# Kernel tuning notes

Measured on AMD Instinct MI355X. Metric: run time of the kernel, lower is better.

Reference implementation:

```python
import jax, jax.numpy as jnp
import numpy as np

NUM_V = 20000
N_EDGES = 160000
IN_CH, OUT_CH = 16, 32
IN_ORDER = OUT_ORDER = MID_ORDER = 2
N_RINGS = 2
BAND_LIMIT = 2
NUM_SAMPLES = 7


def build_kernel_basis(n_in, n_out, bl):
    """Equivariant kernel basis [num_bases, 2*bl+1, 2*n_out+1, 2*n_in+1].
    Freq axis layout: [const, cos(t), sin(t), cos(2t), sin(2t), ...] matching precomp."""
    Din, Dout, F = 2 * n_in + 1, 2 * n_out + 1, 2 * bl + 1
    I = np.eye(2)
    E = np.array([[0., -1.], [1., 0.]])   # rotation by pi/2
    S = np.array([[1., 0.], [0., -1.]])   # reflection
    ES = E @ S
    sl = lambda m: slice(0, 1) if m == 0 else slice(2 * m - 1, 2 * m + 1)
    bases = []

    def add(f, cos_blk, sin_blk, m, n):
        if f > bl:
            return
        B = np.zeros((F, Dout, Din))
        if f == 0:
            B[0, sl(m), sl(n)] = cos_blk
        else:
            B[2 * f - 1, sl(m), sl(n)] = cos_blk
            B[2 * f, sl(m), sl(n)] = sin_blk
        bases.append(B)

    for m in range(n_out + 1):
        for n in range(n_in + 1):
            if m == 0 and n == 0:
                add(0, np.ones((1, 1)), None, 0, 0)
            elif n == 0:  # scalar -> order-m pair: R(m t) e1, R(m t) e2
                add(m, np.array([[1.], [0.]]), np.array([[0.], [1.]]), m, 0)
                add(m, np.array([[0.], [1.]]), np.array([[-1.], [0.]]), m, 0)
            elif m == 0:  # order-n pair -> scalar: rows of R(-n t)
                add(n, np.array([[1., 0.]]), np.array([[0., 1.]]), 0, n)
                add(n, np.array([[0., 1.]]), np.array([[-1., 0.]]), 0, n)
            else:
                d = m - n
                f = abs(d)
                sg = 1.0 if d >= 0 else -1.0
                add(f, I, sg * E, m, n)          # R(d t)
                add(f, E, -sg * I, m, n)         # R(d t + pi/2)
                add(m + n, S, ES, m, n)          # R((m+n) t) S
                add(m + n, ES, -S, m, n)         # R((m+n) t + pi/2) S
    return np.stack(bases).astype(np.float32)


def fourier_mats(order, n):
    th = 2 * np.pi * np.arange(n) / n
    cols = [np.ones(n)]
    for m in range(1, order + 1):
        cols += [np.cos(m * th), np.sin(m * th)]
    T = np.stack(cols, 1)                              # [n_samples, 2*order+1]
    scale = np.array([1.0] + [2.0] * (2 * order)) / n
    Tinv = (T * scale).T                               # [2*order+1, n_samples]
    return jnp.asarray(T, jnp.float32), jnp.asarray(Tinv, jnp.float32)


def rep_act(x, alpha, order):
    """Gauge transport: rotate order-m feature pairs by m*alpha. x: [E,C,2*order+1]."""
    parts = [x[:, :, :1]]
    for m in range(1, order + 1):
        c = jnp.cos(m * alpha)[:, None]
        s = jnp.sin(m * alpha)[:, None]
        a, b = x[:, :, 2 * m - 1], x[:, :, 2 * m]
        parts.append(jnp.stack([c * a - s * b, s * a + c * b], axis=-1))
    return jnp.concatenate(parts, axis=-1)


def gem_conv(x, edge_index, precomp, connection, K, W, b, in_order):
    src, dst = edge_index[1], edge_index[0]
    xt = rep_act(x[src], connection, in_order)               # [E, Cin, Din] gather + transport
    wk = jnp.einsum('bfij,broc->froicj', K, W)               # fold basis with ring weights (small)
    t = jnp.einsum('ecj,froicj->efroi', xt, wk)              # per-edge freq/ring responses
    msg = jnp.einsum('efr,efroi->eoi', precomp, t)           # [E, Cout, Dout]
    out = jax.ops.segment_sum(msg, dst, num_segments=NUM_V)  # scatter-add to vertices
    return out.at[:, :, 0].add(b)                            # bias on scalar component


def regular_relu(x, order):
    T, Tinv = fourier_mats(order, NUM_SAMPLES)
    s = jnp.einsum('vcd,sd->vcs', x, T)   # irrep -> regular samples
    return jnp.einsum('vcs,ds->vcd', jax.nn.relu(s), Tinv)


def setup_inputs() -> dict:
    key = jax.random.key(0)
    k = jax.random.split(key, 8)
    nb = build_kernel_basis(IN_ORDER, MID_ORDER, BAND_LIMIT).shape[0]  # 19
    Din = 2 * IN_ORDER + 1
    x = jax.random.normal(k[0], (NUM_V, IN_CH, Din), jnp.float32)
    edge_index = jax.random.randint(k[1], (2, N_EDGES), 0, NUM_V, dtype=jnp.int32)
    precomp = jax.random.normal(k[2], (N_EDGES, 2 * BAND_LIMIT + 1, N_RINGS), jnp.float32)
    connection = jax.random.uniform(k[3], (N_EDGES,), jnp.float32) * (2 * np.pi)
    W1 = jax.random.normal(k[4], (nb, N_RINGS, OUT_CH, IN_CH), jnp.float32) * 0.1
    W2 = jax.random.normal(k[5], (nb, N_RINGS, OUT_CH, OUT_CH), jnp.float32) * 0.05
    W_lin = jax.random.normal(k[6], (OUT_CH, IN_CH), jnp.float32) * 0.1
    zeros = lambda: jnp.zeros((OUT_CH,), jnp.float32)
    return {"x": x, "edge_index": edge_index, "precomp": precomp, "connection": connection,
            "W1": W1, "b1": zeros(), "W2": W2, "b2": zeros(), "W_lin": W_lin, "b_lin": zeros()}


def reference(x, edge_index, precomp, connection, W1, b1, W2, b2, W_lin, b_lin):
    K = jnp.asarray(build_kernel_basis(IN_ORDER, MID_ORDER, BAND_LIMIT))  # orders equal -> shared basis
    y = gem_conv(x, edge_index, precomp, connection, K, W1, b1, IN_ORDER)
    y = regular_relu(y, MID_ORDER)
    y = gem_conv(y, edge_index, precomp, connection, K, W2, b2, MID_ORDER)
    res = jnp.einsum('vcd,oc->vod', x, W_lin) + b_lin[None, :, None]  # 1x1 conv residual
    o = min(y.shape[2], res.shape[2])
    y = y.at[:, :, :o].add(res[:, :, :o])
    return regular_relu(y, OUT_ORDER)
```

## Files before the change

### kernel.cpp

```cpp
#include <hip/hip_runtime.h>
#include <hip/hip_bf16.h>
#include <cstdint>

#define NV     20000
#define NE     160000
#define IC1    16
#define OC     32
#define DIN    5
#define NSLOT  49
#define NOUT   160
struct SlotTables {
    int n;
    int b[64], f[64], i[64], j[64];
    float v[64];
};

constexpr SlotTables make_slots() {
    SlotTables T{};
    float K[19][5][5][5] = {};
    int nb = 0;
    const int BL = 2;
    auto add = [&](int f, const float (*cb)[2], const float (*sb)[2],
                   int m, int n) {
        if (f > BL) return;
        int r0 = (m == 0) ? 0 : (2 * m - 1), nr = (m == 0) ? 1 : 2;
        int c0 = (n == 0) ? 0 : (2 * n - 1), nc = (n == 0) ? 1 : 2;
        for (int a = 0; a < nr; a++)
            for (int bb = 0; bb < nc; bb++) {
                if (f == 0) {
                    K[nb][0][r0 + a][c0 + bb] = cb[a][bb];
                } else {
                    K[nb][2 * f - 1][r0 + a][c0 + bb] = cb[a][bb];
                    K[nb][2 * f    ][r0 + a][c0 + bb] = sb[a][bb];
                }
            }
        nb++;
    };
    const float ONE[2][2]  = {{1, 0}, {0, 0}};
    const float I2[2][2]   = {{1, 0}, {0, 1}};
    const float E2[2][2]   = {{0, -1}, {1, 0}};
    const float S2[2][2]   = {{1, 0}, {0, -1}};
    const float ES2[2][2]  = {{0, 1}, {1, 0}};
    const float NS2[2][2]  = {{-1, 0}, {0, 1}};
    const float C10[2][2]  = {{1, 0}, {0, 0}};
    const float C01[2][2]  = {{0, 0}, {1, 0}};
    const float CM10[2][2] = {{-1, 0}, {0, 0}};
    const float R10[2][2]  = {{1, 0}, {0, 0}};
    const float R01[2][2]  = {{0, 1}, {0, 0}};
    const float RM10[2][2] = {{-1, 0}, {0, 0}};

    for (int m = 0; m <= 2; m++)
        for (int n = 0; n <= 2; n++) {
            if (m == 0 && n == 0) {
                add(0, ONE, ONE, 0, 0);
            } else if (n == 0) {
                add(m, C10, C01, m, 0);
                add(m, C01, CM10, m, 0);
            } else if (m == 0) {
                add(n, R10, R01, 0, n);
                add(n, R01, RM10, 0, n);
            } else {
                int d = m - n;
                int f = d >= 0 ? d : -d;
                float sg = d >= 0 ? 1.f : -1.f;
                const float sgE[2][2]  = {{0, -sg}, {sg, 0}};
                const float msgI[2][2] = {{-sg, 0}, {0, -sg}};
                add(f, I2, sgE, m, n);
                add(f, E2, msgI, m, n);
                add(m + n, S2, ES2, m, n);
                add(m + n, ES2, NS2, m, n);
            }
        }
    T.n = 0;
    for (int i = 0; i < 5; i++)
        for (int b = 0; b < nb; b++)
            for (int f = 0; f < 5; f++)
                for (int j = 0; j < 5; j++)
                    if (K[b][f][i][j] != 0.0f) {
                        T.b[T.n] = b; T.f[T.n] = f; T.i[T.n] = i;
                        T.j[T.n] = j; T.v[T.n] = K[b][f][i][j];
                        T.n++;
                    }
    return T;
}

constexpr SlotTables SL = make_slots();
static_assert(SL.n == NSLOT, "expect 49 kernel-basis nonzeros");

__device__ __forceinline__ uint32_t bf16_rne(float f) {
    uint32_t u = __float_as_uint(f);
    u += 0x7fffu + ((u >> 16) & 1u);
    return u >> 16;
}

typedef __attribute__((ext_vector_type(8))) short bf16x8;
typedef __attribute__((ext_vector_type(4))) float f32x4;

template<int C>
__global__ __launch_bounds__(256) void build_M(const float* __restrict__ W,
                                               float* __restrict__ M) {
    int t = blockIdx.x * 256 + threadIdx.x;
    const int K = C * 50;
    if (t >= K * NOUT) return;
    int n = t % NOUT, k = t / NOUT;
    int o = n / 5, i = n % 5;
    int c = k / 50, r50 = k % 50;
    int j = r50 / 10, q = r50 % 10;
    int f = q >> 1, r = q & 1;
    float acc = 0.f;
    #pragma unroll
    for (int s = 0; s < NSLOT; s++) {
        if (SL.j[s] == j && SL.f[s] == f && SL.i[s] == i)
            acc += SL.v[s] * W[(size_t)((SL.b[s] * 2 + r) * 32 + o) * C + c];
    }
    M[(size_t)k * NOUT + n] = acc;
}

template<int K>
__global__ __launch_bounds__(256) void build_Mfrag(const float* __restrict__ M,
                                                   uint32_t* __restrict__ Mf) {
    int t = blockIdx.x * 256 + threadIdx.x;
    const int total = (K / 32) * 10 * 64 * 4;
    if (t >= total) return;
    int a = t & 3;
    int idx = t >> 2;
    int lane = idx & 63; idx >>= 6;
    int nt = idx % 10;
    int ck = idx / 10;
    int col = nt * 16 + (lane & 15);
    int k0 = ck * 32 + (lane >> 4) * 8 + 2 * a;
    uint32_t lo = bf16_rne(M[(size_t)k0 * NOUT + col]);
    uint32_t hi = bf16_rne(M[(size_t)(k0 + 1) * NOUT + col]);
    Mf[t] = lo | (hi << 16);
}

__global__ __launch_bounds__(256) void hist_k(const int* __restrict__ ei,
                                              int* __restrict__ counts) {
    int e = blockIdx.x * 256 + threadIdx.x;
    if (e < NE) atomicAdd(&counts[ei[e]], 1);
}

__global__ __launch_bounds__(1024) void scan_k(const int* __restrict__ counts,
                                               int* __restrict__ cursor) {
    __shared__ int part[1024];
    int t = threadIdx.x;
    int base = t * 20;
    int local[20];
    int s = 0;
    #pragma unroll
    for (int k = 0; k < 20; k++) {
        int idx = base + k;
        int c = (idx < NV) ? counts[idx] : 0;
        local[k] = c; s += c;
    }
    part[t] = s;
    __syncthreads();
    for (int off = 1; off < 1024; off <<= 1) {
        int add = (t >= off) ? part[t - off] : 0;
        __syncthreads();
        part[t] += add;
        __syncthreads();
    }
    int run = (t == 0) ? 0 : part[t - 1];
    #pragma unroll
    for (int k = 0; k < 20; k++) {
        int idx = base + k;
        if (idx < NV) { cursor[idx] = run; run += local[k]; }
    }
}

__global__ __launch_bounds__(256) void scatter_k(const int* __restrict__ ei,
                                                 int* __restrict__ cursor,
                                                 int* __restrict__ order) {
    int e = blockIdx.x * 256 + threadIdx.x;
    if (e >= NE) return;
    int pos = atomicAdd(&cursor[ei[e]], 1);
    order[pos] = e;
}

template<int C>
__global__ __launch_bounds__(256) void zbuild(const float* __restrict__ xin,
                                              const int*   __restrict__ ei,
                                              const float* __restrict__ pre,
                                              const float* __restrict__ conn,
                                              const int* __restrict__ cursor,
                                              const int* __restrict__ order,
                                              uint32_t* __restrict__ Z,
                                              int v0, int v1) {
    __shared__ uint32_t st[6400];
    int tid = threadIdx.x;
    int t = blockIdx.x * 256 + tid;
    int rows = (v1 - v0) * C;
    bool valid = (t < rows);
    int c = t % C;
    int v = v0 + t / C;
    int beg = 0, end = 0;
    if (valid) { beg = (v == 0) ? 0 : cursor[v - 1]; end = cursor[v]; }
    float acc[50];
    #pragma unroll
    for (int z = 0; z < 50; z++) acc[z] = 0.f;

    for (int k = beg; k < end; k++) {
        int e = order[k];
        int src = ei[NE + e];
        float al = conn[e];
        float c1 = __cosf(al), s1 = __sinf(al);
        float c2 = c1 * c1 - s1 * s1, s2 = 2.0f * c1 * s1;
        float p[10];
        #pragma unroll
        for (int q = 0; q < 10; q++) p[q] = pre[(size_t)e * 10 + q];
        const float* xb = xin + ((size_t)src * C + c) * DIN;
        float x0 = xb[0], x1 = xb[1], x2 = xb[2], x3 = xb[3], x4 = xb[4];
        float xt[5];
        xt[0] = x0;
        xt[1] = c1 * x1 - s1 * x2;
        xt[2] = s1 * x1 + c1 * x2;
        xt[3] = c2 * x3 - s2 * x4;
        xt[4] = s2 * x3 + c2 * x4;
        #pragma unroll
        for (int j = 0; j < 5; j++)
            #pragma unroll
            for (int q = 0; q < 10; q++)
                acc[j * 10 + q] = fmaf(xt[j], p[q], acc[j * 10 + q]);
    }
    uint32_t* sb = st + tid * 25;
    #pragma unroll
    for (int z = 0; z < 25; z++)
        sb[z] = bf16_rne(acc[2 * z]) | (bf16_rne(acc[2 * z + 1]) << 16);
    __syncthreads();
    size_t gbase = (size_t)blockIdx.x * 6400;
    int rbase = blockIdx.x * 256;
    for (int i = tid; i < 6400; i += 256) {
        if (rbase + i / 25 < rows) Z[gbase + i] = st[i];
    }
}

template<int K>
__global__ __launch_bounds__(256) void gemm_mfma(const uint32_t* __restrict__ Z,
                                                 const uint32_t* __restrict__ Mf,
                                                 float* __restrict__ Y,
                                                 int rows) {
    constexpr int NC = K / 32;
    __shared__ uint4 Bs[2][640];
    int t = threadIdx.x;
    int lane = t & 63;
    int wave = t >> 6;
    int r0 = blockIdx.x * 64 + wave * 16;
    int mrow = lane & 15;
    int q = lane >> 4;
    int ra = r0 + mrow;
    if (ra >= rows) ra = rows - 1;
    const uint32_t* za = Z + (size_t)ra * (K / 2) + q * 4;
    const uint4* mfg = (const uint4*)Mf + lane;

    auto stage = [&](int ck, int nb) {
        const uint4* gp = mfg + (size_t)ck * 640;
        for (int i = wave; i < 10; i += 4)
            __builtin_amdgcn_global_load_lds(
                (const __attribute__((address_space(1))) void*)(gp + i * 64),
                (__attribute__((address_space(3))) void*)(&Bs[nb][i * 64]),
                16, 0, 0);
    };

    f32x4 acc[10];
    #pragma unroll
    for (int nt = 0; nt < 10; nt++) acc[nt] = {0.f, 0.f, 0.f, 0.f};

    stage(0, 0);
    bf16x8 af = *(const bf16x8*)za;
    __syncthreads();

    for (int ck = 0; ck < NC; ck++) {
        int buf = ck & 1;
        bf16x8 af_n = af;
        if (ck + 1 < NC) {
            stage(ck + 1, buf ^ 1);
            af_n = *(const bf16x8*)(za + (ck + 1) * 16);
        }
        bf16x8 bf[10];
        #pragma unroll
        for (int nt = 0; nt < 10; nt++)
            bf[nt] = *(const bf16x8*)&Bs[buf][nt * 64 + lane];
        #pragma unroll
        for (int nt = 0; nt < 10; nt++)
            acc[nt] = __builtin_amdgcn_mfma_f32_16x16x32_bf16(af, bf[nt],
                                                              acc[nt], 0, 0, 0);
        af = af_n;
        __syncthreads();
    }
    #pragma unroll
    for (int reg = 0; reg < 4; reg++) {
        int rr = r0 + q * 4 + reg;
        if (rr < rows) {
            float* yb = Y + (size_t)rr * NOUT + (lane & 15);
            #pragma unroll
            for (int nt = 0; nt < 10; nt++) yb[nt * 16] = acc[nt][reg];
        }
    }
}

__device__ __forceinline__ void fourier_relu(float d0, float d1, float d2,
                                             float d3, float d4, float* out5) {
    float o0 = 0, o1 = 0, o2 = 0, o3 = 0, o4 = 0;
    #pragma unroll
    for (int k = 0; k < 7; k++) {
        float th = (float)k * (6.28318530717958647692f / 7.0f);
        float ck = __cosf(th), sk = __sinf(th);
        float c2k = ck * ck - sk * sk, s2k = 2.f * ck * sk;
        float sv = d0 + ck * d1 + sk * d2 + c2k * d3 + s2k * d4;
        sv = fmaxf(sv, 0.f);
        o0 += sv; o1 += sv * ck; o2 += sv * sk; o3 += sv * c2k; o4 += sv * s2k;
    }
    const float i7 = 1.0f / 7.0f;
    out5[0] = o0 * i7; out5[1] = o1 * (2.f * i7); out5[2] = o2 * (2.f * i7);
    out5[3] = o3 * (2.f * i7); out5[4] = o4 * (2.f * i7);
}

__global__ __launch_bounds__(256) void relu_mid(float* __restrict__ y,
                                                const float* __restrict__ b1) {
    int t = blockIdx.x * 256 + threadIdx.x;
    if (t >= NV * 32) return;
    int ch = t & 31;
    float* yb = y + (size_t)t * 5;
    float r[5];
    fourier_relu(yb[0] + b1[ch], yb[1], yb[2], yb[3], yb[4], r);
    #pragma unroll
    for (int d = 0; d < 5; d++) yb[d] = r[d];
}

__global__ __launch_bounds__(256) void final_k(const float* __restrict__ y2,
                                               const float* __restrict__ x,
                                               const float* __restrict__ Wl,
                                               const float* __restrict__ bl,
                                               const float* __restrict__ b2,
                                               float* __restrict__ out) {
    int t = blockIdx.x * 256 + threadIdx.x;
    if (t >= NV * 32) return;
    int o = t & 31;
    int v = t >> 5;
    float r0 = 0, r1 = 0, r2 = 0, r3 = 0, r4 = 0;
    const float* xb = x + (size_t)v * (IC1 * DIN);
    const float* wl = Wl + o * IC1;
    #pragma unroll
    for (int c = 0; c < IC1; c++) {
        float w = wl[c];
        r0 = fmaf(w, xb[c*5+0], r0); r1 = fmaf(w, xb[c*5+1], r1);
        r2 = fmaf(w, xb[c*5+2], r2); r3 = fmaf(w, xb[c*5+3], r3);
        r4 = fmaf(w, xb[c*5+4], r4);
    }
    float blo = bl[o];
    const float* yb = y2 + (size_t)t * 5;
    float d0 = yb[0] + b2[o] + r0 + blo;
    float d1 = yb[1] + r1 + blo;
    float d2 = yb[2] + r2 + blo;
    float d3 = yb[3] + r3 + blo;
    float d4 = yb[4] + r4 + blo;
    float r[5];
    fourier_relu(d0, d1, d2, d3, d4, r);
    float* ob = out + (size_t)t * 5;
    #pragma unroll
    for (int d = 0; d < 5; d++) ob[d] = r[d];
}

extern "C" void kernel_launch(void* const* d_in, const int* in_sizes, int n_in,
                              void* d_out, int out_size, void* d_ws, size_t ws_size,
                              hipStream_t stream) {
    const float* x    = (const float*)d_in[0];
    const int*   ei   = (const int*)  d_in[1];
    const float* pre  = (const float*)d_in[2];
    const float* conn = (const float*)d_in[3];
    const float* W1   = (const float*)d_in[4];
    const float* b1   = (const float*)d_in[5];
    const float* W2   = (const float*)d_in[6];
    const float* b2   = (const float*)d_in[7];
    const float* Wl   = (const float*)d_in[8];
    const float* bl   = (const float*)d_in[9];
    float* out = (float*)d_out;

    const int K1 = IC1 * 50;
    const int K2 = OC  * 50;

    const size_t Y_BYTES   = (size_t)NV * NOUT * sizeof(float);
    const size_t M1_BYTES  = (size_t)K1 * NOUT * sizeof(float);
    const size_t M2_BYTES  = (size_t)K2 * NOUT * sizeof(float);
    const size_t MF1_BYTES = (size_t)(K1 / 32) * 10 * 64 * 16;
    const size_t MF2_BYTES = (size_t)(K2 / 32) * 10 * 64 * 16;
    const size_t CSR_BYTES = (size_t)(2 * NV + NE) * sizeof(int);
    char* ws = (char*)d_ws;
    float* y1 = (float*)(ws);
    float* y2 = (float*)(ws + Y_BYTES);
    float* M1 = (float*)(ws + 2 * Y_BYTES);
    float* M2 = (float*)(ws + 2 * Y_BYTES + M1_BYTES);
    uint32_t* Mf1 = (uint32_t*)(ws + 2 * Y_BYTES + M1_BYTES + M2_BYTES);
    uint32_t* Mf2 = (uint32_t*)(ws + 2 * Y_BYTES + M1_BYTES + M2_BYTES + MF1_BYTES);
    int* counts = (int*)(ws + 2 * Y_BYTES + M1_BYTES + M2_BYTES + MF1_BYTES + MF2_BYTES);
    int* cursor = counts + NV;
    int* order  = cursor + NV;
    size_t fixed = 2 * Y_BYTES + M1_BYTES + M2_BYTES + MF1_BYTES + MF2_BYTES
                 + CSR_BYTES;

    size_t tail = (ws_size > fixed) ? (ws_size - fixed) : 0;
    uint32_t* zbuf;
    size_t zcap;
    if (tail >= Y_BYTES) { zbuf = (uint32_t*)(ws + fixed); zcap = tail; }
    else                 { zbuf = (uint32_t*)d_out;        zcap = Y_BYTES; }
    int chunk1 = (int)(zcap / ((size_t)K1 * 2)); if (chunk1 > NV) chunk1 = NV;
    int chunk2 = (int)(zcap / ((size_t)K2 * 2)); if (chunk2 > NV) chunk2 = NV;

    hipMemsetAsync(counts, 0, NV * sizeof(int), stream);

    build_M<IC1><<<(K1 * NOUT + 255) / 256, 256, 0, stream>>>(W1, M1);
    build_M<OC> <<<(K2 * NOUT + 255) / 256, 256, 0, stream>>>(W2, M2);
    build_Mfrag<K1><<<((K1 / 32) * 2560 + 255) / 256, 256, 0, stream>>>(M1, Mf1);
    build_Mfrag<K2><<<((K2 / 32) * 2560 + 255) / 256, 256, 0, stream>>>(M2, Mf2);

    hist_k   <<<(NE + 255) / 256, 256, 0, stream>>>(ei, counts);
    scan_k   <<<1, 1024, 0, stream>>>(counts, cursor);
    scatter_k<<<(NE + 255) / 256, 256, 0, stream>>>(ei, cursor, order);

    for (int v0 = 0; v0 < NV; v0 += chunk1) {
        int v1 = v0 + chunk1; if (v1 > NV) v1 = NV;
        int rows = v1 - v0;
        zbuild<IC1><<<(rows * IC1 + 255) / 256, 256, 0, stream>>>(
            x, ei, pre, conn, cursor, order, zbuf, v0, v1);
        gemm_mfma<K1><<<(rows + 63) / 64, 256, 0, stream>>>(
            zbuf, Mf1, y1 + (size_t)v0 * NOUT, rows);
    }
    relu_mid<<<(NV * 32 + 255) / 256, 256, 0, stream>>>(y1, b1);
    for (int v0 = 0; v0 < NV; v0 += chunk2) {
        int v1 = v0 + chunk2; if (v1 > NV) v1 = NV;
        int rows = v1 - v0;
        zbuild<OC><<<(rows * OC + 255) / 256, 256, 0, stream>>>(
            y1, ei, pre, conn, cursor, order, zbuf, v0, v1);
        gemm_mfma<K2><<<(rows + 63) / 64, 256, 0, stream>>>(
            zbuf, Mf2, y2 + (size_t)v0 * NOUT, rows);
    }
    final_k<<<(NV * 32 + 255) / 256, 256, 0, stream>>>(y2, x, Wl, bl, b2, out);
}
```

Before: 274.1 us.

## Pack sorted edge records and split edge loop across thread pairs with prefetch

Adds an edge_pack kernel that writes each edge's source index, cos/sin of the connection angle and precomp coefficients into a contiguous, destination-sorted record array. The z-building kernel then reads these packed records directly instead of chasing order->ei/pre/conn, and computes no trig per channel. Each (vertex, channel) row is now split between two threads that take alternating edges and combine results with a lane shuffle. The loop also software-prefetches the next edge's record and features. This costs an extra pre-pass kernel and workspace, and doubles the thread count with higher register pressure.

New measurement: 383.5 us. 39.9% more time.

```diff
diff --git a/kernel.cpp b/kernel.cpp
--- a/kernel.cpp
+++ b/kernel.cpp
@@ -178,61 +178,110 @@
     order[pos] = e;
 }
 
+__global__ __launch_bounds__(256) void edge_pack(const int* __restrict__ ei,
+                                                 const float* __restrict__ pre,
+                                                 const float* __restrict__ conn,
+                                                 const int* __restrict__ order,
+                                                 int* __restrict__ SRC,
+                                                 float4* __restrict__ REC) {
+    int k = blockIdx.x * 256 + threadIdx.x;
+    if (k > NE) return;
+    if (k == NE) {
+        SRC[NE] = 0;
+        REC[(size_t)NE * 3 + 0] = float4{0.f, 0.f, 0.f, 0.f};
+        REC[(size_t)NE * 3 + 1] = float4{0.f, 0.f, 0.f, 0.f};
+        REC[(size_t)NE * 3 + 2] = float4{0.f, 0.f, 0.f, 0.f};
+        return;
+    }
+    int e = order[k];
+    SRC[k] = ei[NE + e];
+    float al = conn[e];
+    float c1 = __cosf(al), s1 = __sinf(al);
+    const float* pp = pre + (size_t)e * 10;
+    REC[(size_t)k * 3 + 0] = float4{c1, s1, pp[0], pp[1]};
+    REC[(size_t)k * 3 + 1] = float4{pp[2], pp[3], pp[4], pp[5]};
+    REC[(size_t)k * 3 + 2] = float4{pp[6], pp[7], pp[8], pp[9]};
+}
+
 template<int C>
-__global__ __launch_bounds__(256) void zbuild(const float* __restrict__ xin,
-                                              const int*   __restrict__ ei,
-                                              const float* __restrict__ pre,
-                                              const float* __restrict__ conn,
-                                              const int* __restrict__ cursor,
-                                              const int* __restrict__ order,
-                                              uint32_t* __restrict__ Z,
-                                              int v0, int v1) {
-    __shared__ uint32_t st[6400];
+__global__ __launch_bounds__(256) void zbuild2(const float* __restrict__ xin,
+                                               const int*   __restrict__ SRC,
+                                               const float4* __restrict__ REC,
+                                               const int* __restrict__ cursor,
+                                               uint32_t* __restrict__ Z,
+                                               int v0, int v1) {
+    __shared__ uint32_t st[3200];
     int tid = threadIdx.x;
     int t = blockIdx.x * 256 + tid;
-    int rows = (v1 - v0) * C;
-    bool valid = (t < rows);
-    int c = t % C;
-    int v = v0 + t / C;
-    int beg = 0, end = 0;
-    if (valid) { beg = (v == 0) ? 0 : cursor[v - 1]; end = cursor[v]; }
+    int pair = t >> 1, h = t & 1;
+    int rows = v1 - v0;
+    int vl = pair / C;
+    int c = pair % C;
+    bool tvalid = vl < rows;
+    int v = v0 + (tvalid ? vl : rows - 1);
+    int beg = (v == 0) ? 0 : cursor[v - 1];
+    int end = cursor[v];
+    if (!tvalid) end = beg;
+
     float acc[50];
     #pragma unroll
     for (int z = 0; z < 50; z++) acc[z] = 0.f;
 
-    for (int k = beg; k < end; k++) {
-        int e = order[k];
-        int src = ei[NE + e];
-        float al = conn[e];
-        float c1 = __cosf(al), s1 = __sinf(al);
-        float c2 = c1 * c1 - s1 * s1, s2 = 2.0f * c1 * s1;
-        float p[10];
-        #pragma unroll
-        for (int q = 0; q < 10; q++) p[q] = pre[(size_t)e * 10 + q];
-        const float* xb = xin + ((size_t)src * C + c) * DIN;
+    int k = beg + h;
+    if (k < end) {
+        int kn = (k + 2 < end) ? k + 2 : NE;
+        int sC = SRC[k];
+        int sN = SRC[kn];
+        const float4* rp = REC + (size_t)k * 3;
+        float4 r0 = rp[0], r1 = rp[1], r2 = rp[2];
+        const float* xb = xin + ((size_t)sC * C + c) * DIN;
         float x0 = xb[0], x1 = xb[1], x2 = xb[2], x3 = xb[3], x4 = xb[4];
-        float xt[5];
-        xt[0] = x0;
-        xt[1] = c1 * x1 - s1 * x2;
-        xt[2] = s1 * x1 + c1 * x2;
-        xt[3] = c2 * x3 - s2 * x4;
-        xt[4] = s2 * x3 + c2 * x4;
-        #pragma unroll
-        for (int j = 0; j < 5; j++)
+        while (true) {
+            bool more = (k + 2 < end);
+            int kn2 = (k + 4 < end) ? k + 4 : NE;
+            int sN2 = SRC[kn2];
+            const float* xbn = xin + ((size_t)sN * C + c) * DIN;
+            float y0 = xbn[0], y1 = xbn[1], y2 = xbn[2], y3 = xbn[3],
+                  y4 = xbn[4];
+            const float4* rpn = REC + (size_t)kn * 3;
+            float4 n0 = rpn[0], n1 = rpn[1], n2 = rpn[2];
+            float c1 = r0.x, s1 = r0.y;
+            float c2 = c1 * c1 - s1 * s1, s2 = 2.f * c1 * s1;
+            float xt[5];
+            xt[0] = x0;
+            xt[1] = c1 * x1 - s1 * x2;
+            xt[2] = s1 * x1 + c1 * x2;
+            xt[3] = c2 * x3 - s2 * x4;
+            xt[4] = s2 * x3 + c2 * x4;
+            float p[10] = {r0.z, r0.w, r1.x, r1.y, r1.z, r1.w,
+                           r2.x, r2.y, r2.z, r2.w};
             #pragma unroll
-            for (int q = 0; q < 10; q++)
-                acc[j * 10 + q] = fmaf(xt[j], p[q], acc[j * 10 + q]);
-    }
-    uint32_t* sb = st + tid * 25;
-    #pragma unroll
-    for (int z = 0; z < 25; z++)
-        sb[z] = bf16_rne(acc[2 * z]) | (bf16_rne(acc[2 * z + 1]) << 16);
+            for (int j = 0; j < 5; j++)
+                #pragma unroll
+                for (int q = 0; q < 10; q++)
+                    acc[j * 10 + q] = fmaf(xt[j], p[q], acc[j * 10 + q]);
+            if (!more) break;
+            k += 2;
+            r0 = n0; r1 = n1; r2 = n2;
+            x0 = y0; x1 = y1; x2 = y2; x3 = y3; x4 = y4;
+            sN = sN2; kn = kn2;
+        }
+    }
+    #pragma unroll
+    for (int z = 0; z < 50; z++) acc[z] += __shfl_xor(acc[z], 1);
+    uint32_t* sb = st + (tid >> 1) * 25;
+    #pragma unroll
+    for (int uu = 0; uu < 13; uu++) {
+        int u = uu * 2 + h;
+        if (u < 25)
+            sb[u] = bf16_rne(acc[2 * u]) | (bf16_rne(acc[2 * u + 1]) << 16);
+    }
     __syncthreads();
-    size_t gbase = (size_t)blockIdx.x * 6400;
-    int rbase = blockIdx.x * 256;
-    for (int i = tid; i < 6400; i += 256) {
-        if (rbase + i / 25 < rows) Z[gbase + i] = st[i];
-    }
+    size_t gbase = (size_t)blockIdx.x * 3200;
+    int pbase = blockIdx.x * 128;
+    int totp = rows * C;
+    for (int i = tid; i < 3200; i += 256)
+        if (pbase + i / 25 < totp) Z[gbase + i] = st[i];
 }
 
 template<int K>
@@ -386,6 +435,8 @@
     const size_t MF1_BYTES = (size_t)(K1 / 32) * 10 * 64 * 16;
     const size_t MF2_BYTES = (size_t)(K2 / 32) * 10 * 64 * 16;
     const size_t CSR_BYTES = (size_t)(2 * NV + NE) * sizeof(int);
+    const size_t REC_BYTES = (size_t)(NE + 1) * 48;
+    const size_t SRC_BYTES = (((size_t)(NE + 1) * 4 + 15) / 16) * 16;
     char* ws = (char*)d_ws;
     float* y1 = (float*)(ws);
     float* y2 = (float*)(ws + Y_BYTES);
@@ -396,8 +447,11 @@
     int* counts = (int*)(ws + 2 * Y_BYTES + M1_BYTES + M2_BYTES + MF1_BYTES + MF2_BYTES);
     int* cursor = counts + NV;
     int* order  = cursor + NV;
-    size_t fixed = 2 * Y_BYTES + M1_BYTES + M2_BYTES + MF1_BYTES + MF2_BYTES
-                 + CSR_BYTES;
+    size_t csr_end = 2 * Y_BYTES + M1_BYTES + M2_BYTES + MF1_BYTES + MF2_BYTES
+                   + CSR_BYTES;
+    float4* REC = (float4*)(ws + csr_end);
+    int*    SRC = (int*)(ws + csr_end + REC_BYTES);
+    size_t fixed = csr_end + REC_BYTES + SRC_BYTES;
 
     size_t tail = (ws_size > fixed) ? (ws_size - fixed) : 0;
     uint32_t* zbuf;
@@ -417,12 +471,14 @@
     hist_k   <<<(NE + 255) / 256, 256, 0, stream>>>(ei, counts);
     scan_k   <<<1, 1024, 0, stream>>>(counts, cursor);
     scatter_k<<<(NE + 255) / 256, 256, 0, stream>>>(ei, cursor, order);
+    edge_pack<<<(NE + 256) / 256, 256, 0, stream>>>(ei, pre, conn, order,
+                                                    SRC, REC);
 
     for (int v0 = 0; v0 < NV; v0 += chunk1) {
         int v1 = v0 + chunk1; if (v1 > NV) v1 = NV;
         int rows = v1 - v0;
-        zbuild<IC1><<<(rows * IC1 + 255) / 256, 256, 0, stream>>>(
-            x, ei, pre, conn, cursor, order, zbuf, v0, v1);
+        zbuild2<IC1><<<((size_t)rows * IC1 * 2 + 255) / 256, 256, 0, stream>>>(
+            x, SRC, REC, cursor, zbuf, v0, v1);
         gemm_mfma<K1><<<(rows + 63) / 64, 256, 0, stream>>>(
             zbuf, Mf1, y1 + (size_t)v0 * NOUT, rows);
     }
@@ -430,8 +486,8 @@
     for (int v0 = 0; v0 < NV; v0 += chunk2) {
         int v1 = v0 + chunk2; if (v1 > NV) v1 = NV;
         int rows = v1 - v0;
-        zbuild<OC><<<(rows * OC + 255) / 256, 256, 0, stream>>>(
-            y1, ei, pre, conn, cursor, order, zbuf, v0, v1);
+        zbuild2<OC><<<((size_t)rows * OC * 2 + 255) / 256, 256, 0, stream>>>(
+            y1, SRC, REC, cursor, zbuf, v0, v1);
         gemm_mfma<K2><<<(rows + 63) / 64, 256, 0, stream>>>(
             zbuf, Mf2, y2 + (size_t)v0 * NOUT, rows);
     }
```
